# Kernel tuning notes

Measured on AMD Instinct MI355X. Metric: run time of the kernel, lower is better.

Reference implementation:

```python
import jax, jax.numpy as jnp
import numpy as np

C = 96          # num_features
G = 3           # deform / weight groups
K = 9           # 3x3 kernel taps
OFF_CH = G * 3 * K  # 81: offset-conv output channels


def conv3x3(x, w, b=None):
    out = jax.lax.conv_general_dilated(
        x, w, window_strides=(1, 1), padding=((1, 1), (1, 1)),
        dimension_numbers=('NCHW', 'OIHW', 'NCHW'))
    if b is not None:
        out = out + b[None, :, None, None]
    return out


def offset_gen(x):
    o1, o2, m = jnp.split(x, 3, axis=1)
    return jnp.concatenate([o1, o2], axis=1), jax.nn.sigmoid(m)


def dcn(x, offset, mask, w, b):
    # Modulated deformable conv (DCNv2): offset = [y-offsets (G*K ch), x-offsets (G*K ch)]
    N, Cx, H, W = x.shape
    Cg = Cx // G
    GK = G * K
    dy = offset[:, :GK].reshape(N, G, K, H, W)
    dx = offset[:, GK:].reshape(N, G, K, H, W)
    m = mask.reshape(N, G, K, H, W)
    ky = (jnp.arange(K) // 3 - 1).astype(x.dtype)
    kx = (jnp.arange(K) % 3 - 1).astype(x.dtype)
    # sampling positions: p = p0 + kernel_offset + learned_offset (stride 1, pad 1)
    py = dy + jnp.arange(H, dtype=x.dtype)[:, None] + ky[:, None, None]   # [N,G,K,H,W]
    px = dx + jnp.arange(W, dtype=x.dtype) + kx[:, None, None]
    y0 = jnp.floor(py)
    x0 = jnp.floor(px)
    xf = x.reshape(N, G, Cg, H * W)
    gather = jax.vmap(jax.vmap(lambda xg, ig: xg[:, ig]))  # ([Cg,HW],[KHW]) -> [Cg,KHW]
    val = jnp.zeros((N, G, Cg, K, H, W), x.dtype)
    for cy, cx in ((y0, x0), (y0, x0 + 1), (y0 + 1, x0), (y0 + 1, x0 + 1)):
        wgt = (1 - jnp.abs(py - cy)) * (1 - jnp.abs(px - cx))
        valid = (cy >= 0) & (cy <= H - 1) & (cx >= 0) & (cx <= W - 1)
        iy = jnp.clip(cy, 0, H - 1).astype(jnp.int32)
        ix = jnp.clip(cx, 0, W - 1).astype(jnp.int32)
        idx = (iy * W + ix).reshape(N, G, K * H * W)
        g = gather(xf, idx).reshape(N, G, Cg, K, H, W)
        val = val + g * (wgt * valid.astype(x.dtype))[:, :, None]
    val = val * m[:, :, None]                       # modulation
    wg = w.reshape(G, Cx // G, Cg, K)               # grouped weight [G, Cout/G, Cin/G, K]
    out = jnp.einsum('ngckhw,gock->ngohw', val, wg).reshape(N, Cx, H, W)
    return out + b[None, :, None, None]


def setup_inputs() -> dict:
    key = jax.random.key(0)
    ks = jax.random.split(key, 16)
    B, H, W = 2, 128, 128
    d = {
        'X1': jax.random.normal(ks[0], (B, C, H, W), jnp.float32),
        'X2': jax.random.normal(ks[1], (B, C, H, W), jnp.float32),
        'w_bot': jax.random.normal(ks[2], (C, 2 * C, 3, 3), jnp.float32) * 0.02,
    }
    for i in range(4):
        d[f'w_off{i+1}'] = jax.random.normal(ks[3 + i], (OFF_CH, C, 3, 3), jnp.float32) * 0.02
        d[f'w_d{i+1}'] = jax.random.normal(ks[7 + i], (C, C // G, 3, 3), jnp.float32) * 0.05
        d[f'b_d{i+1}'] = jax.random.normal(ks[11 + i], (C,), jnp.float32) * 0.01
    return d


def reference(X1, X2, w_bot, w_off1, w_off2, w_off3, w_off4,
              w_d1, b_d1, w_d2, b_d2, w_d3, b_d3, w_d4, b_d4):
    B, Cx, H, W = X1.shape
    # frames: f0 = cat(X1, X1), f1 = cat(X1, X2) along channels, flattened to (B*2, 2C, H, W)
    feat = jnp.stack([jnp.concatenate([X1, X1], axis=1),
                      jnp.concatenate([X1, X2], axis=1)], axis=1)
    feat = feat.reshape(B * 2, 2 * Cx, H, W)
    feat = conv3x3(feat, w_bot)
    for w_off, w_d, b_d in ((w_off1, w_d1, b_d1), (w_off2, w_d2, b_d2),
                            (w_off3, w_d3, b_d3), (w_off4, w_d4, b_d4)):
        off, m = offset_gen(conv3x3(feat, w_off))
        feat = dcn(feat, off, m, w_d, b_d)
    return feat[1:2]


if __name__ == '__main__':
    out = reference(**setup_inputs())
    print(out.shape)
```

## Files before the change

### kernel.cpp

```cpp
#include <hip/hip_runtime.h>

#define HW 16384
#define RSB 130

typedef short short8 __attribute__((ext_vector_type(8)));
typedef float f32x4 __attribute__((ext_vector_type(4)));
typedef unsigned short ushort8v __attribute__((ext_vector_type(8)));

__device__ __forceinline__ float b2f(unsigned short u) {
    return __uint_as_float(((unsigned)u) << 16);
}
__device__ __forceinline__ unsigned short f2b(float f) {
    unsigned u = __float_as_uint(f);
    return (unsigned short)((u + 0x7fffu + ((u >> 16) & 1u)) >> 16);
}

__global__ __launch_bounds__(256) void prep_all(
    const float* __restrict__ X1, const float* __restrict__ X2,
    const float* __restrict__ w_bot,
    const float* __restrict__ wo0, const float* __restrict__ wo1,
    const float* __restrict__ wo2, const float* __restrict__ wo3,
    const float* __restrict__ wd0, const float* __restrict__ wd1,
    const float* __restrict__ wd2, const float* __restrict__ wd3,
    unsigned short* __restrict__ wBbot, unsigned short* __restrict__ wBoff,
    unsigned short* __restrict__ wdB,  unsigned short* __restrict__ in_nhwc,
    unsigned short* __restrict__ featA, unsigned short* __restrict__ featB) {
    const int N0 = 165888, N1 = N0 + 331776, N2 = N1 + 110592,
              N3 = N2 + 393216, N4 = N3 + 24768;
    for (int idx = blockIdx.x * 256 + threadIdx.x; idx < N4; idx += 131072) {
        if (idx < N0) {
            int i = idx;
            int v = i & 7, lane = (i >> 3) & 63, t = i >> 9;
            int kc = t % 6; t /= 6;
            int tap = t % 9, nt = t / 9;
            int oc = nt * 16 + (lane & 15), cin = kc * 32 + (lane >> 4) * 8 + v;
            wBbot[i] = f2b(oc < 96 ? w_bot[(oc * 192 + cin) * 9 + tap] : 0.f);
        } else if (idx < N1) {
            int j = idx - N0;
            int l = j / 82944, i = j - l * 82944;
            const float* w = l == 0 ? wo0 : l == 1 ? wo1 : l == 2 ? wo2 : wo3;
            int v = i & 7, lane = (i >> 3) & 63, t = i >> 9;
            int kc = t % 3; t /= 3;
            int tap = t % 9, nt = t / 9;
            int oc = nt * 16 + (lane & 15), cin = kc * 32 + (lane >> 4) * 8 + v;
            wBoff[j] = f2b(oc < 81 ? w[(oc * 96 + cin) * 9 + tap] : 0.f);
        } else if (idx < N2) {
            int j = idx - N1;
            int l = j / 27648, i = j - l * 27648;
            const float* w = l == 0 ? wd0 : l == 1 ? wd1 : l == 2 ? wd2 : wd3;
            int v = i & 7, lane = (i >> 3) & 63, t = i >> 9;
            int nt = t & 1; t >>= 1;
            int tap = t % 9, g = t / 9;
            int oc = nt * 16 + (lane & 15), c = (lane >> 4) * 8 + v;
            wdB[j] = f2b(w[((g * 32 + oc) * 32 + c) * 9 + tap]);
        } else if (idx < N3) {
            int j = idx - N2;
            int cb = j >> 14, p = j & (HW - 1);
            int ch = cb * 8;
            int y = p >> 7, x = p & 127;
            ushort8v o;
#pragma unroll
            for (int q = 0; q < 8; ++q) {
                int c = ch + q;
                float v = (c < 96) ? X1[c * HW + p] : X2[(c - 96) * HW + p];
                o[q] = f2b(v);
            }
            *(ushort8v*)(in_nhwc + (size_t)((y + 1) * RSB + (x + 1)) * 192 + ch) = o;
        } else {
            int j = idx - N3;
            int bp = j / 48, c8 = j - bp * 48;
            int y, x;
            if (bp < 130)      { y = 0;   x = bp; }
            else if (bp < 260) { y = 129; x = bp - 130; }
            else { int t2 = bp - 260; y = 1 + (t2 >> 1); x = (t2 & 1) ? 129 : 0; }
            size_t pix = (size_t)y * RSB + x;
            ushort8v z = {0, 0, 0, 0, 0, 0, 0, 0};
            if (c8 < 24)      *(ushort8v*)(in_nhwc + pix * 192 + c8 * 8) = z;
            else if (c8 < 36) *(ushort8v*)(featA + pix * 96 + (c8 - 24) * 8) = z;
            else              *(ushort8v*)(featB + pix * 96 + (c8 - 36) * 8) = z;
        }
    }
}

__global__ __launch_bounds__(256) void conv_bot(const unsigned short* __restrict__ in,
                                                const unsigned short* __restrict__ wB,
                                                unsigned short* __restrict__ outb) {
    const int tid = threadIdx.x;
    const int lane = tid & 63;
    const int wid = tid >> 6;
    const int msub = wid & 1, nh = wid >> 1;
    const int pbase = blockIdx.x * 32 + msub * 16;
    const int p = pbase + (lane & 15);
    const int y = p >> 7, x = p & 127;
    const int klane = lane >> 4;
    const unsigned short* arow = in + (size_t)((y + 1) * RSB + (x + 1)) * 192 + klane * 8;
    const unsigned short* wb = wB + (size_t)(nh * 3) * 9 * 6 * 512 + lane * 8;

    f32x4 a0 = {0.f, 0.f, 0.f, 0.f};
    f32x4 a1 = {0.f, 0.f, 0.f, 0.f};
    f32x4 a2 = {0.f, 0.f, 0.f, 0.f};
#pragma unroll
    for (int tap = 0; tap < 9; ++tap) {
        const unsigned short* at = arow + ((tap / 3 - 1) * RSB + (tap % 3 - 1)) * 192;
#pragma unroll
        for (int kc = 0; kc < 6; ++kc) {
            short8 a  = *(const short8*)(at + kc * 32);
            short8 b0 = *(const short8*)(wb + ((0 * 9 + tap) * 6 + kc) * 512);
            short8 b1 = *(const short8*)(wb + ((1 * 9 + tap) * 6 + kc) * 512);
            short8 b2 = *(const short8*)(wb + ((2 * 9 + tap) * 6 + kc) * 512);
            a0 = __builtin_amdgcn_mfma_f32_16x16x32_bf16(a, b0, a0, 0, 0, 0);
            a1 = __builtin_amdgcn_mfma_f32_16x16x32_bf16(a, b1, a1, 0, 0, 0);
            a2 = __builtin_amdgcn_mfma_f32_16x16x32_bf16(a, b2, a2, 0, 0, 0);
        }
    }
    const int col = lane & 15;
#pragma unroll
    for (int r = 0; r < 4; ++r) {
        int pr = pbase + klane * 4 + r;
        int yy = pr >> 7, xx = pr & 127;
        size_t base = (size_t)((yy + 1) * RSB + (xx + 1)) * 96;
        outb[base + (nh * 3 + 0) * 16 + col] = f2b(a0[r]);
        outb[base + (nh * 3 + 1) * 16 + col] = f2b(a1[r]);
        outb[base + (nh * 3 + 2) * 16 + col] = f2b(a2[r]);
    }
}

__global__ __launch_bounds__(512) void offdcn_kernel(
    const unsigned short* __restrict__ feat,
    const unsigned short* __restrict__ wBoff,
    const unsigned short* __restrict__ wdB,
    const float* __restrict__ b_d,
    void* __restrict__ outp, int last) {
    __shared__ float s_off[64][97];

    const int tid = threadIdx.x;
    const int lane = tid & 63;
    const int w = tid >> 6;
    const int col = lane & 15, klane = lane >> 4;
    const int pb = ((blockIdx.x & 7) << 5) + (blockIdx.x >> 3);
    const int P0 = pb * 64;

    {
        const int pf = w >> 1, nh = w & 1;
        const int p = P0 + pf * 16 + col;
        const int y = p >> 7, x = p & 127;
        const unsigned short* arow = feat + (size_t)((y + 1) * RSB + (x + 1)) * 96 + klane * 8;
        const unsigned short* wb = wBoff + (size_t)(nh * 3) * 9 * 3 * 512 + lane * 8;

        f32x4 a0 = {0.f, 0.f, 0.f, 0.f};
        f32x4 a1 = {0.f, 0.f, 0.f, 0.f};
        f32x4 a2 = {0.f, 0.f, 0.f, 0.f};
#pragma unroll
        for (int tap = 0; tap < 9; ++tap) {
            const unsigned short* at = arow + ((tap / 3 - 1) * RSB + (tap % 3 - 1)) * 96;
#pragma unroll
            for (int kc = 0; kc < 3; ++kc) {
                short8 a  = *(const short8*)(at + kc * 32);
                short8 b0 = *(const short8*)(wb + ((0 * 9 + tap) * 3 + kc) * 512);
                short8 b1 = *(const short8*)(wb + ((1 * 9 + tap) * 3 + kc) * 512);
                short8 b2 = *(const short8*)(wb + ((2 * 9 + tap) * 3 + kc) * 512);
                a0 = __builtin_amdgcn_mfma_f32_16x16x32_bf16(a, b0, a0, 0, 0, 0);
                a1 = __builtin_amdgcn_mfma_f32_16x16x32_bf16(a, b1, a1, 0, 0, 0);
                a2 = __builtin_amdgcn_mfma_f32_16x16x32_bf16(a, b2, a2, 0, 0, 0);
            }
        }
#pragma unroll
        for (int r = 0; r < 4; ++r) {
            int pl = pf * 16 + klane * 4 + r;
            s_off[pl][nh * 48 + 0 * 16 + col] = a0[r];
            s_off[pl][nh * 48 + 1 * 16 + col] = a1[r];
            s_off[pl][nh * 48 + 2 * 16 + col] = a2[r];
        }
    }
    __syncthreads();

    for (int sidx = w; sidx < 12; sidx += 8) {
        const int pf = sidx & 3, g = sidx >> 2;
        const int p = P0 + pf * 16 + col;
        const int y = p >> 7, x = p & 127;
        const int pl = pf * 16 + col;
        const int coct = klane * 8;

        const unsigned short* fgc = feat + g * 32 + coct;
        const unsigned short* wb = wdB + (size_t)g * 9 * 2 * 512 + lane * 8;

        int adr[9][4];
        float wgt[9][4];
#pragma unroll
        for (int k = 0; k < 9; ++k) {
            float dy = s_off[pl][g * 9 + k];
            float dx = s_off[pl][27 + g * 9 + k];
            float mr = s_off[pl][54 + g * 9 + k];
            float m = 1.f / (1.f + __expf(-mr));

            float py = dy + (float)y + (float)(k / 3 - 1);
            float px = dx + (float)x + (float)(k % 3 - 1);
            float y0f = floorf(py), x0f = floorf(px);
            float fy = py - y0f, fx = px - x0f;

            float vy0 = (y0f >= 0.f   && y0f <= 127.f) ? 1.f : 0.f;
            float vy1 = (y0f >= -1.f  && y0f <= 126.f) ? 1.f : 0.f;
            float vx0 = (x0f >= 0.f   && x0f <= 127.f) ? 1.f : 0.f;
            float vx1 = (x0f >= -1.f  && x0f <= 126.f) ? 1.f : 0.f;

            int iy0r = (int)y0f, ix0r = (int)x0f;
            int iy0 = min(max(iy0r, 0), 127);
            int iy1 = min(max(iy0r + 1, 0), 127);
            int ix0 = min(max(ix0r, 0), 127);
            int ix1 = min(max(ix0r + 1, 0), 127);

            wgt[k][0] = (1.f - fy) * (1.f - fx) * vy0 * vx0 * m;
            wgt[k][1] = (1.f - fy) * fx        * vy0 * vx1 * m;
            wgt[k][2] = fy        * (1.f - fx) * vy1 * vx0 * m;
            wgt[k][3] = fy        * fx         * vy1 * vx1 * m;

            adr[k][0] = (iy0 + 1) * RSB + ix0 + 1;
            adr[k][1] = (iy0 + 1) * RSB + ix1 + 1;
            adr[k][2] = (iy1 + 1) * RSB + ix0 + 1;
            adr[k][3] = (iy1 + 1) * RSB + ix1 + 1;
        }

        f32x4 acc0 = {0.f, 0.f, 0.f, 0.f};
        f32x4 acc1 = {0.f, 0.f, 0.f, 0.f};

        ushort8v ga[4], gb[4], gc[4];
#define LDG(buf, kk) { \
        buf[0] = *(const ushort8v*)(fgc + (size_t)adr[kk][0] * 96); \
        buf[1] = *(const ushort8v*)(fgc + (size_t)adr[kk][1] * 96); \
        buf[2] = *(const ushort8v*)(fgc + (size_t)adr[kk][2] * 96); \
        buf[3] = *(const ushort8v*)(fgc + (size_t)adr[kk][3] * 96); }
#define CMP(buf, kk) { \
        short8 a; \
        _Pragma("unroll") for (int j = 0; j < 8; ++j) { \
            float val = wgt[kk][0] * b2f(buf[0][j]) + wgt[kk][1] * b2f(buf[1][j]) \
                      + wgt[kk][2] * b2f(buf[2][j]) + wgt[kk][3] * b2f(buf[3][j]); \
            a[j] = (short)f2b(val); } \
        short8 b0 = *(const short8*)(wb + ((kk) * 2 + 0) * 512); \
        short8 b1 = *(const short8*)(wb + ((kk) * 2 + 1) * 512); \
        acc0 = __builtin_amdgcn_mfma_f32_16x16x32_bf16(a, b0, acc0, 0, 0, 0); \
        acc1 = __builtin_amdgcn_mfma_f32_16x16x32_bf16(a, b1, acc1, 0, 0, 0); }

        LDG(ga, 0); LDG(gb, 1); LDG(gc, 2);
        CMP(ga, 0); LDG(ga, 3);
        CMP(gb, 1); LDG(gb, 4);
        CMP(gc, 2); LDG(gc, 5);
        CMP(ga, 3); LDG(ga, 6);
        CMP(gb, 4); LDG(gb, 7);
        CMP(gc, 5); LDG(gc, 8);
        CMP(ga, 6); CMP(gb, 7); CMP(gc, 8);
#undef LDG
#undef CMP

#pragma unroll
        for (int r = 0; r < 4; ++r) {
            int pr = P0 + pf * 16 + klane * 4 + r;
            int ch0 = g * 32 + col, ch1 = g * 32 + 16 + col;
            float o0 = acc0[r] + b_d[ch0];
            float o1 = acc1[r] + b_d[ch1];
            if (!last) {
                int yy = pr >> 7, xx = pr & 127;
                unsigned short* fo = (unsigned short*)outp;
                size_t base = (size_t)((yy + 1) * RSB + (xx + 1)) * 96;
                fo[base + ch0] = f2b(o0);
                fo[base + ch1] = f2b(o1);
            } else {
                float* fo = (float*)outp;
                fo[(size_t)ch0 * HW + pr] = o0;
                fo[(size_t)ch1 * HW + pr] = o1;
            }
        }
    }
}

extern "C" void kernel_launch(void* const* d_in, const int* in_sizes, int n_in,
                              void* d_out, int out_size, void* d_ws, size_t ws_size,
                              hipStream_t stream) {
    const float* X1    = (const float*)d_in[0];
    const float* X2    = (const float*)d_in[1];
    const float* w_bot = (const float*)d_in[2];
    const float* wo0 = (const float*)d_in[3],  *wo1 = (const float*)d_in[6],
               *wo2 = (const float*)d_in[9],  *wo3 = (const float*)d_in[12];
    const float* wd0 = (const float*)d_in[4],  *wd1 = (const float*)d_in[7],
               *wd2 = (const float*)d_in[10], *wd3 = (const float*)d_in[13];
    const float* bd[4] = {(const float*)d_in[5], (const float*)d_in[8],
                          (const float*)d_in[11], (const float*)d_in[14]};

    unsigned short* in_nhwc = (unsigned short*)d_ws;
    unsigned short* featA   = in_nhwc + 3244800;
    unsigned short* featB   = featA + 1622400;
    unsigned short* wBbot   = featB + 1622400;
    unsigned short* wBoff   = wBbot + 165888;
    unsigned short* wdB     = wBoff + 4 * 82944;

    prep_all<<<512, 256, 0, stream>>>(X1, X2, w_bot, wo0, wo1, wo2, wo3,
                                      wd0, wd1, wd2, wd3,
                                      wBbot, wBoff, wdB, in_nhwc, featA, featB);
    conv_bot<<<512, 256, 0, stream>>>(in_nhwc, wBbot, featA);

    unsigned short* cur = featA;
    unsigned short* nxt = featB;
    for (int it = 0; it < 4; ++it) {
        void* outp = (it == 3) ? d_out : (void*)nxt;
        offdcn_kernel<<<256, 512, 0, stream>>>(cur, wBoff + it * 82944,
                                               wdB + it * 27648, bd[it],
                                               outp, it == 3 ? 1 : 0);
        unsigned short* t = cur; cur = nxt; nxt = t;
    }
}
```

Measured before the change: 119.0 us.

## Halve offdcn block tile and use padded border instead of bounds masks

The fused offset-conv plus deformable-conv kernel now uses 256-thread blocks covering 32 pixels, launched as 512 blocks instead of 256 blocks of 512 threads covering 64 pixels. This spreads work over more, smaller blocks and halves the shared offset buffer. The per-tap validity masks are removed: sample indices are clamped into the zero-padded 130-wide buffer, so out-of-range taps read zeros. This relies on the padding ring staying zero. The bilinear blend is also written as explicit fmaf chains.

```diff
diff --git a/kernel.cpp b/kernel.cpp
--- a/kernel.cpp
+++ b/kernel.cpp
@@ -125,20 +125,20 @@
     }
 }
 
-__global__ __launch_bounds__(512) void offdcn_kernel(
+__global__ __launch_bounds__(256) void offdcn_kernel(
     const unsigned short* __restrict__ feat,
     const unsigned short* __restrict__ wBoff,
     const unsigned short* __restrict__ wdB,
     const float* __restrict__ b_d,
     void* __restrict__ outp, int last) {
-    __shared__ float s_off[64][97];
+    __shared__ float s_off[32][97];
 
     const int tid = threadIdx.x;
     const int lane = tid & 63;
     const int w = tid >> 6;
     const int col = lane & 15, klane = lane >> 4;
-    const int pb = ((blockIdx.x & 7) << 5) + (blockIdx.x >> 3);
-    const int P0 = pb * 64;
+    const int pb = ((blockIdx.x & 7) << 6) + (blockIdx.x >> 3);
+    const int P0 = pb * 32;
 
     {
         const int pf = w >> 1, nh = w & 1;
@@ -174,8 +174,8 @@
     }
     __syncthreads();
 
-    for (int sidx = w; sidx < 12; sidx += 8) {
-        const int pf = sidx & 3, g = sidx >> 2;
+    for (int sidx = w; sidx < 6; sidx += 4) {
+        const int pf = sidx & 1, g = sidx >> 1;
         const int p = P0 + pf * 16 + col;
         const int y = p >> 7, x = p & 127;
         const int pl = pf * 16 + col;
@@ -197,27 +197,23 @@
             float px = dx + (float)x + (float)(k % 3 - 1);
             float y0f = floorf(py), x0f = floorf(px);
             float fy = py - y0f, fx = px - x0f;
-
-            float vy0 = (y0f >= 0.f   && y0f <= 127.f) ? 1.f : 0.f;
-            float vy1 = (y0f >= -1.f  && y0f <= 126.f) ? 1.f : 0.f;
-            float vx0 = (x0f >= 0.f   && x0f <= 127.f) ? 1.f : 0.f;
-            float vx1 = (x0f >= -1.f  && x0f <= 126.f) ? 1.f : 0.f;
-
-            int iy0r = (int)y0f, ix0r = (int)x0f;
-            int iy0 = min(max(iy0r, 0), 127);
-            int iy1 = min(max(iy0r + 1, 0), 127);
-            int ix0 = min(max(ix0r, 0), 127);
-            int ix1 = min(max(ix0r + 1, 0), 127);
-
-            wgt[k][0] = (1.f - fy) * (1.f - fx) * vy0 * vx0 * m;
-            wgt[k][1] = (1.f - fy) * fx        * vy0 * vx1 * m;
-            wgt[k][2] = fy        * (1.f - fx) * vy1 * vx0 * m;
-            wgt[k][3] = fy        * fx         * vy1 * vx1 * m;
-
-            adr[k][0] = (iy0 + 1) * RSB + ix0 + 1;
-            adr[k][1] = (iy0 + 1) * RSB + ix1 + 1;
-            adr[k][2] = (iy1 + 1) * RSB + ix0 + 1;
-            adr[k][3] = (iy1 + 1) * RSB + ix1 + 1;
+            float gy = 1.f - fy, gx = 1.f - fx;
+
+            int py0 = (int)y0f + 1, px0 = (int)x0f + 1;
+            int iy0 = min(max(py0, 0), 129);
+            int iy1 = min(max(py0 + 1, 0), 129);
+            int ix0 = min(max(px0, 0), 129);
+            int ix1 = min(max(px0 + 1, 0), 129);
+
+            wgt[k][0] = gy * gx * m;
+            wgt[k][1] = gy * fx * m;
+            wgt[k][2] = fy * gx * m;
+            wgt[k][3] = fy * fx * m;
+
+            adr[k][0] = iy0 * RSB + ix0;
+            adr[k][1] = iy0 * RSB + ix1;
+            adr[k][2] = iy1 * RSB + ix0;
+            adr[k][3] = iy1 * RSB + ix1;
         }
 
         f32x4 acc0 = {0.f, 0.f, 0.f, 0.f};
@@ -232,8 +228,10 @@
 #define CMP(buf, kk) { \
         short8 a; \
         _Pragma("unroll") for (int j = 0; j < 8; ++j) { \
-            float val = wgt[kk][0] * b2f(buf[0][j]) + wgt[kk][1] * b2f(buf[1][j]) \
-                      + wgt[kk][2] * b2f(buf[2][j]) + wgt[kk][3] * b2f(buf[3][j]); \
+            float val = fmaf(wgt[kk][0], b2f(buf[0][j]), \
+                        fmaf(wgt[kk][1], b2f(buf[1][j]), \
+                        fmaf(wgt[kk][2], b2f(buf[2][j]), \
+                             wgt[kk][3] * b2f(buf[3][j])))); \
             a[j] = (short)f2b(val); } \
         short8 b0 = *(const short8*)(wb + ((kk) * 2 + 0) * 512); \
         short8 b1 = *(const short8*)(wb + ((kk) * 2 + 1) * 512); \
@@ -301,7 +299,7 @@
     unsigned short* nxt = featB;
     for (int it = 0; it < 4; ++it) {
         void* outp = (it == 3) ? d_out : (void*)nxt;
-        offdcn_kernel<<<256, 512, 0, stream>>>(cur, wBoff + it * 82944,
+        offdcn_kernel<<<512, 256, 0, stream>>>(cur, wBoff + it * 82944,
                                                wdB + it * 27648, bd[it],
                                                outp, it == 3 ? 1 : 0);
         unsigned short* t = cur; cur = nxt; nxt = t;
```

Result: slower. 122.6 us (median of 2 runs) (+3.1%).
